# Kernel tuning notes

Hardware: AMD Instinct MI355X
Metric: run time of the kernel (lower is better)

Reference implementation:

```python
import jax, jax.numpy as jnp
import numpy as np

N = 512    # nnodes
H = 8      # attention heads
C = 32     # gnn_repr_size (per head)
ER = 32    # edge_repr_size
FE = 3     # feat_emb_size
E = 16384  # edges (avg degree 32)


def gat_conv(x, edge_index, edge_attr, W, att_src, att_dst, We, att_edge, b):
    """PyG GATConv (edge_dim=1, concat=True, add_self_loops=True, eval mode)."""
    n = x.shape[0]
    h_, c_ = att_src.shape
    row, col = edge_index[0], edge_index[1]
    # self loops with fill_value='mean': mean of incoming edge_attr per target node
    deg = jax.ops.segment_sum(jnp.ones_like(edge_attr), col, num_segments=n)
    loop_attr = jax.ops.segment_sum(edge_attr, col, num_segments=n) / jnp.maximum(deg, 1.0)
    ar = jnp.arange(n)
    row = jnp.concatenate([row, ar])
    col = jnp.concatenate([col, ar])
    ea = jnp.concatenate([edge_attr, loop_attr])
    # node projections [n, H, C]
    h = (x @ W.T).reshape(n, h_, c_)
    a_src = jnp.sum(h * att_src, axis=-1)  # [n, H]
    a_dst = jnp.sum(h * att_dst, axis=-1)  # [n, H]
    e = (ea[:, None] @ We.T).reshape(-1, h_, c_)  # [E', H, C]
    a_e = jnp.sum(e * att_edge, axis=-1)          # [E', H]
    alpha = jax.nn.leaky_relu(a_src[row] + a_dst[col] + a_e, 0.2)
    # softmax over edges grouped by destination node
    amax = jax.ops.segment_max(alpha, col, num_segments=n)
    ex = jnp.exp(alpha - amax[col])
    denom = jax.ops.segment_sum(ex, col, num_segments=n)
    alpha = ex / (denom[col] + 1e-16)
    out = jax.ops.segment_sum(h[row] * alpha[..., None], col, num_segments=n)
    return out.reshape(n, h_ * c_) + b


def setup_inputs():
    key = jax.random.key(0)
    ks = jax.random.split(key, 24)
    s = 0.05
    HC = H * C
    in_len = N * ER + 3 * N + 3 * FE  # combiner1 input length
    return {
        "dist": jax.random.uniform(ks[0], (N, N), dtype=jnp.float32),
        "markov": jax.random.uniform(ks[1], (N, N), dtype=jnp.float32),
        "demand": jax.random.normal(ks[2], (N,), dtype=jnp.float32),
        "W_week": jax.random.normal(ks[3], (7, FE)) * s,
        "W_cap": jax.random.normal(ks[4], (26, FE)) * s,
        "W_veh": jax.random.normal(ks[5], (15, FE)) * s,
        "g1_W": jax.random.normal(ks[6], (HC, 1)) * s,
        "g1_att_src": jax.random.normal(ks[7], (H, C)) * s,
        "g1_att_dst": jax.random.normal(ks[8], (H, C)) * s,
        "g1_We": jax.random.normal(ks[9], (HC, 1)) * s,
        "g1_att_edge": jax.random.normal(ks[10], (H, C)) * s,
        "g1_b": jnp.zeros((HC,), dtype=jnp.float32),
        "g2_W": jax.random.normal(ks[11], (HC, HC)) * s,
        "g2_att_src": jax.random.normal(ks[12], (H, C)) * s,
        "g2_att_dst": jax.random.normal(ks[13], (H, C)) * s,
        "g2_We": jax.random.normal(ks[14], (HC, 1)) * s,
        "g2_att_edge": jax.random.normal(ks[15], (H, C)) * s,
        "g2_b": jnp.zeros((HC,), dtype=jnp.float32),
        "Wes": jax.random.normal(ks[16], (ER, 2 * HC)) * s,
        "bes": jnp.zeros((ER,), dtype=jnp.float32),
        "Wc1": jax.random.normal(ks[17], (N, in_len)) * 0.01,
        "bc1": jnp.zeros((N,), dtype=jnp.float32),
        "Wc2": jax.random.normal(ks[18], (N, N)) * s,
        "bc2": jnp.zeros((N,), dtype=jnp.float32),
        "stops": jax.random.randint(ks[19], (256,), 0, N),
        "edge_index": jax.random.randint(ks[20], (2, E), 0, N),
        "weekday": 3,
        "vehicles": 7,
        "capacity": 12,
    }


def reference(dist, markov, demand, W_week, W_cap, W_veh,
              g1_W, g1_att_src, g1_att_dst, g1_We, g1_att_edge, g1_b,
              g2_W, g2_att_src, g2_att_dst, g2_We, g2_att_edge, g2_b,
              Wes, bes, Wc1, bc1, Wc2, bc2,
              stops, edge_index, weekday, vehicles, capacity):
    n = dist.shape[0]
    dist = (dist - dist.min()) / (dist.max() - dist.min())
    x = demand[:, None]  # [n, 1]
    ea = markov[edge_index[0], edge_index[1]]  # [E]
    x = jax.nn.relu(gat_conv(x, edge_index, ea, g1_W, g1_att_src, g1_att_dst, g1_We, g1_att_edge, g1_b))
    x = jax.nn.relu(gat_conv(x, edge_index, ea, g2_W, g2_att_src, g2_att_dst, g2_We, g2_att_edge, g2_b))
    HC_ = x.shape[1]
    # all-pairs edge representation: concat(x[i], x[j]) over meshgrid -> [n*n, 2*HC]
    er = jnp.concatenate([
        jnp.broadcast_to(x[:, None, :], (n, n, HC_)),
        jnp.broadcast_to(x[None, :, :], (n, n, HC_)),
    ], axis=-1).reshape(n * n, 2 * HC_)
    er = (er @ Wes.T + bes).reshape(n, -1)  # [n, n*ER]
    week = jnp.broadcast_to(W_week[weekday], (n, W_week.shape[1]))
    cap = jnp.broadcast_to(W_cap[capacity], (n, W_cap.shape[1]))
    veh = jnp.broadcast_to(W_veh[vehicles], (n, W_veh.shape[1]))
    stop = jnp.broadcast_to(jnp.zeros((n,), dtype=dist.dtype).at[stops].set(1.0)[None, :], (n, n))
    feat = jnp.concatenate([er, dist, markov, week, cap, veh, stop], axis=1)
    out = jax.nn.relu(feat @ Wc1.T + bc1) @ Wc2.T + bc2
    return out
```

## Files before the change

### kernel.cpp

```cpp
#include <hip/hip_runtime.h>
#include <hip/hip_bf16.h>

typedef __hip_bfloat16 bf16;
typedef __attribute__((ext_vector_type(8))) short bf16x8;
typedef __attribute__((ext_vector_type(4))) float f32x4;

#define NNODE 512
#define NEDGE 16384
#define INLEN 17929
#define K1P   1088

#define WS_EA      0
#define WS_CSRC    16384
#define WS_CEA     32768
#define WS_DEG     49152
#define WS_STARTS  49664
#define WS_LATTR   50176
#define WS_MM      50688
#define WS_MMP     50690
#define WS_STOPV   50818
#define WS_AE      51330
#define WS_PS      51346
#define WS_H       55552
#define WS_G2WT    186624
#define WS_H2      317696
#define WS_ASRC    448768
#define WS_ADST    452864
#define WS_UV      456960
#define WS_K       489728
#define WS_APACK   490240
#define WS_BPACK   768768
#define WS_OUT1    1047296
#define WS_WC2B    1178368
#define WS_WESF    1309440
#define WS_ASRC2   1325824
#define WS_ADST2   1329920
#define WS_CURSOR  1334016
#define WS_DEGP    1334528
#define WS_LSUMP   1367296
#define WS_OUT1F   1400064

static __device__ __forceinline__ unsigned short f2bfbits(float x){
  bf16 b = __float2bfloat16(x);
  union { bf16 b; unsigned short u; } c; c.b = b; return c.u;
}

__global__ __launch_bounds__(256)
void k_prep(const float* __restrict__ demand, const float* __restrict__ W1,
            const float* __restrict__ att_s, const float* __restrict__ att_d,
            const int* __restrict__ stops, const float* __restrict__ Wes,
            const float* __restrict__ dist, const float* __restrict__ markov,
            const int* __restrict__ eidx,
            const float* __restrict__ g1We, const float* __restrict__ g1ae,
            const float* __restrict__ g2We, const float* __restrict__ g2ae,
            const float* __restrict__ g2W,  const float* __restrict__ g2as,
            const float* __restrict__ g2ad, const float* __restrict__ Wc2,
            float* __restrict__ outp, float* ws){
  int b = blockIdx.x, tid = threadIdx.x;
  if (b < 512){
    int hd = tid>>5, c = tid&31;
    float hv = demand[b] * W1[tid];
    ws[WS_H + b*256 + tid] = hv;
    float ps = hv * att_s[tid];
    float pd = hv * att_d[tid];
    for (int off=16; off; off>>=1){ ps += __shfl_down(ps,off,32); pd += __shfl_down(pd,off,32); }
    if (c==0){ ws[WS_ASRC + b*8+hd]=ps; ws[WS_ADST + b*8+hd]=pd; }
  } else if (b == 512){
    ws[WS_STOPV+tid] = 0.f; ws[WS_STOPV+256+tid] = 0.f;
    __syncthreads();
    ws[WS_STOPV + stops[tid]] = 1.0f;
    if (tid < 8){
      float s=0.f; for (int c=0;c<32;c++) s += g1We[tid*32+c]*g1ae[tid*32+c];
      ws[WS_AE+tid]=s;
    } else if (tid < 16){
      int h=tid-8; float s=0.f; for (int c=0;c<32;c++) s += g2We[h*32+c]*g2ae[h*32+c];
      ws[WS_AE+8+h]=s;
    }
  } else if (b < 515){
    for (int idx = (b-513)*8192 + tid; idx < (b-512)*8192; idx += 256){
      int k = idx>>8, c = idx&255;
      ws[WS_WESF+idx] = (k<32) ? Wes[k*512+c] : Wes[(k-32)*512+256+c];
    }
  } else if (b < 579){
    __shared__ float smn[256], smx[256];
    int p = b-515;
    float mn = 3.4e38f, mx = -3.4e38f;
    const float4* dv = (const float4*)(dist + p*4096);
    #pragma unroll
    for (int k=0;k<4;k++){
      float4 v = dv[k*256 + tid];
      mn = fminf(mn, fminf(fminf(v.x,v.y), fminf(v.z,v.w)));
      mx = fmaxf(mx, fmaxf(fmaxf(v.x,v.y), fmaxf(v.z,v.w)));
    }
    smn[tid]=mn; smx[tid]=mx; __syncthreads();
    for (int off=128; off; off>>=1){
      if (tid<off){ smn[tid]=fminf(smn[tid],smn[tid+off]); smx[tid]=fmaxf(smx[tid],smx[tid+off]); }
      __syncthreads();
    }
    if (tid==0){ ws[WS_MMP+p]=smn[0]; ws[WS_MMP+64+p]=smx[0]; }
  } else if (b < 643){
    __shared__ int   hd_[512];
    __shared__ float hf_[512];
    int k = b-579;
    hd_[tid]=0; hd_[256+tid]=0; hf_[tid]=0.f; hf_[256+tid]=0.f;
    __syncthreads();
    int e = k*256 + tid;
    int r = eidx[e], c = eidx[NEDGE+e];
    float a = markov[r*NNODE + c];
    ws[WS_EA+e] = a;
    atomicAdd(&hd_[c], 1);
    atomicAdd(&hf_[c], a);
    __syncthreads();
    ((int*)(ws+WS_DEGP))[k*512+tid]     = hd_[tid];
    ((int*)(ws+WS_DEGP))[k*512+256+tid] = hd_[256+tid];
    ws[WS_LSUMP + k*512+tid]     = hf_[tid];
    ws[WS_LSUMP + k*512+256+tid] = hf_[256+tid];
  } else if (b < 659){
    int j = b-643;
    const float* att = (j<8) ? g2as : g2ad;
    int h = j&7;
    float s = 0.f;
    for (int c=0;c<32;c++) s += att[h*32+c] * g2W[(h*32+c)*256 + tid];
    ws[WS_PS + j*256 + tid] = s;
  } else if (b < 675){
    __shared__ float T[64][65];
    int tb = b-659, tr = tb>>2, tc = tb&3;
    int w = tid>>6, c = tid&63;
    for (int k=0;k<16;k++){
      int r = k*4 + w;
      T[r][c] = g2W[(tr*64+r)*256 + tc*64 + c];
    }
    __syncthreads();
    for (int k=0;k<16;k++){
      int r = k*4 + w;
      ws[WS_G2WT + (tc*64+r)*256 + tr*64 + c] = T[c][r];
    }
  } else if (b == 675){
    ((int*)(ws+WS_CURSOR))[tid] = 0;
    ((int*)(ws+WS_CURSOR))[256+tid] = 0;
  } else if (b < 740){
    int blk = b - 676;
    const float4* src = (const float4*)(Wc2 + blk*4096);
    ushort4* dst = (ushort4*)((unsigned short*)(ws+WS_WC2B) + blk*4096);
    #pragma unroll
    for (int i=0;i<4;i++){
      float4 v = src[i*256+tid];
      ushort4 u;
      u.x = f2bfbits(v.x); u.y = f2bfbits(v.y);
      u.z = f2bfbits(v.z); u.w = f2bfbits(v.w);
      dst[i*256+tid] = u;
    }
  } else {
    int blk = b - 740;
    float4 z = {0.f,0.f,0.f,0.f};
    float4* o1f = (float4*)(ws + WS_OUT1F);
    float4* op  = (float4*)outp;
    o1f[blk*512 + tid] = z;
    o1f[blk*512 + 256 + tid] = z;
    op[blk*512 + tid] = z;
    op[blk*512 + 256 + tid] = z;
  }
}

__global__ __launch_bounds__(512)
void k_scansc(const int* __restrict__ eidx, float* ws){
  __shared__ int sc[512];
  __shared__ int startS[512];
  __shared__ float rmn[64], rmx[64];
  int t = threadIdx.x, b = blockIdx.x;
  const int* dp = (const int*)(ws+WS_DEGP);
  int d = 0;
  for (int k=0;k<64;k++) d += dp[k*512+t];
  sc[t] = d; __syncthreads();
  for (int off=1; off<512; off<<=1){
    int v = (t>=off) ? sc[t-off] : 0; __syncthreads();
    sc[t] += v; __syncthreads();
  }
  startS[t] = sc[t]-d;
  if (b == 0){
    float l = 0.f;
    for (int k=0;k<64;k++) l += ws[WS_LSUMP+k*512+t];
    ((int*)(ws+WS_STARTS))[t] = startS[t];
    ((int*)(ws+WS_DEG))[t] = d;
    ws[WS_LATTR+t] = l / (float)(d>1 ? d : 1);
    if (t < 64){ rmn[t]=ws[WS_MMP+t]; rmx[t]=ws[WS_MMP+64+t]; }
    __syncthreads();
    if (t == 0){
      float mn=rmn[0], mx=rmx[0];
      for (int i=1;i<64;i++){ mn=fminf(mn,rmn[i]); mx=fmaxf(mx,rmx[i]); }
      ws[WS_MM]=mn; ws[WS_MM+1]=mx;
    }
  }
  __syncthreads();
  int e = b*512 + t;
  int c = eidx[NEDGE+e];
  int p = startS[c] + atomicAdd((int*)(ws+WS_CURSOR)+c, 1);
  ((int*)(ws+WS_CSRC))[p] = eidx[e];
  ws[WS_CEA+p] = ws[WS_EA+e];
}

template<int MODE>
__global__ __launch_bounds__(256)
void k_agg(const float* __restrict__ hbuf, const float* __restrict__ asrc,
           const float* __restrict__ adst, const int* __restrict__ csrc,
           const float* __restrict__ cea, const int* __restrict__ starts,
           const int* __restrict__ deg, const float* __restrict__ lattr,
           const float* __restrict__ AEp, const float* __restrict__ bvec,
           const float* __restrict__ dist, const float* __restrict__ markov,
           float* ws){
  int t = blockIdx.x, tid = threadIdx.x, hd = tid>>5;
  __shared__ int   srcE[256];
  __shared__ float eaE[256];
  __shared__ float Lall[256*8];
  __shared__ float AE[8], mh[8], dh[8], sw[8];
  __shared__ float xrow[256], uvrow[64];
  if (tid<8) AE[tid]=AEp[tid];
  __syncthreads();
  int d = deg[t], s0 = starts[t];
  if (d > 256) d = 256;
  for (int e=tid; e<d; e+=256){ srcE[e]=csrc[s0+e]; eaE[e]=cea[s0+e]; }
  __syncthreads();
  {
    int h8 = tid&7;
    float adt = adst[t*8+h8], aeh = AE[h8];
    for (int e = tid>>3; e < d; e += 32){
      float a = asrc[srcE[e]*8+h8] + adt + eaE[e]*aeh;
      Lall[e*8+h8] = a>=0.f ? a : 0.2f*a;
    }
  }
  __syncthreads();
  {
    int h = tid>>5, j = tid&31;
    float aself = asrc[t*8+h] + adst[t*8+h] + lattr[t]*AE[h];
    aself = aself>=0.f ? aself : 0.2f*aself;
    float mm = aself;
    for (int e=j; e<d; e+=32) mm = fmaxf(mm, Lall[e*8+h]);
    for (int off=16; off; off>>=1) mm = fmaxf(mm, __shfl_down(mm,off,32));
    mm = __shfl(mm, 0, 32);
    float dd = 0.f;
    for (int e=j; e<d; e+=32) dd += __expf(Lall[e*8+h]-mm);
    for (int off=16; off; off>>=1) dd += __shfl_down(dd,off,32);
    if (j==0){
      float se = __expf(aself-mm);
      mh[h]=mm; dh[h]=dd+se+1e-16f; sw[h]=se;
    }
  }
  __syncthreads();
  {
    int h8 = tid&7;
    for (int e = tid>>3; e < d; e += 32)
      Lall[e*8+h8] = __expf(Lall[e*8+h8] - mh[h8]);
  }
  __syncthreads();
  float a0 = sw[hd]*hbuf[t*256+tid], a1=0.f, a2=0.f, a3=0.f, a4=0.f, a5=0.f, a6=0.f, a7=0.f;
  int e = 0;
  for (; e+8<=d; e+=8){
    a0 += Lall[(e+0)*8+hd]*hbuf[srcE[e+0]*256+tid];
    a1 += Lall[(e+1)*8+hd]*hbuf[srcE[e+1]*256+tid];
    a2 += Lall[(e+2)*8+hd]*hbuf[srcE[e+2]*256+tid];
    a3 += Lall[(e+3)*8+hd]*hbuf[srcE[e+3]*256+tid];
    a4 += Lall[(e+4)*8+hd]*hbuf[srcE[e+4]*256+tid];
    a5 += Lall[(e+5)*8+hd]*hbuf[srcE[e+5]*256+tid];
    a6 += Lall[(e+6)*8+hd]*hbuf[srcE[e+6]*256+tid];
    a7 += Lall[(e+7)*8+hd]*hbuf[srcE[e+7]*256+tid];
  }
  for (; e<d; e++) a0 += Lall[e*8+hd]*hbuf[srcE[e]*256+tid];
  float v = fmaxf((((a0+a1)+(a2+a3))+((a4+a5)+(a6+a7)))/dh[hd] + bvec[tid], 0.f);
  xrow[tid] = v;
  __syncthreads();
  if (MODE == 1){
    const float* g2wt = ws + WS_G2WT;
    float h0=0.f,h1=0.f,h2=0.f,h3=0.f;
    for (int c=0;c<256;c+=4){
      h0 += xrow[c+0]*g2wt[(c+0)*256+tid];
      h1 += xrow[c+1]*g2wt[(c+1)*256+tid];
      h2 += xrow[c+2]*g2wt[(c+2)*256+tid];
      h3 += xrow[c+3]*g2wt[(c+3)*256+tid];
    }
    ws[WS_H2 + t*256 + tid] = (h0+h1)+(h2+h3);
    if (tid < 64){
      int j = tid>>2, q = tid&3;
      const float* pr = ws + WS_PS + j*256 + q*64;
      const float* xr = xrow + q*64;
      float p = 0.f;
      for (int c=0;c<64;c++) p += xr[c]*pr[c];
      p += __shfl_down(p,2,4);
      p += __shfl_down(p,1,4);
      if (q==0){
        if (j<8) ws[WS_ASRC2 + t*8+j] = p;
        else     ws[WS_ADST2 + t*8+(j-8)] = p;
      }
    }
  } else {
    int k = tid>>2, q = tid&3;
    const float* wr = ws + WS_WESF + k*256 + q*64;
    const float* xr = xrow + q*64;
    float p = 0.f;
    for (int c=0;c<64;c++) p += xr[c]*wr[c];
    p += __shfl_down(p,2,4);
    p += __shfl_down(p,1,4);
    if (q==0){ ws[WS_UV + t*64+k] = p; uvrow[k] = p; }
    __syncthreads();
    float mn = ws[WS_MM], mx = ws[WS_MM+1];
    float inv = 1.0f/(mx-mn);
    bf16* ap = (bf16*)(ws+WS_APACK);
    const float* mrow = markov + t*512;
    for (int j=tid; j<K1P; j+=256){
      float v2;
      if (j<32)        v2 = uvrow[j];
      else if (j<544)  v2 = (dist[t*512 + j-32] - mn) * inv;
      else if (j<1056) v2 = mrow[j-544];
      else             v2 = 0.f;
      ap[(size_t)t*K1P + j] = __float2bfloat16(v2);
    }
  }
}

__global__ __launch_bounds__(1024)
void k_skpack(const float* __restrict__ Wc1, const float* __restrict__ bc1,
              const float* __restrict__ bes, const float* __restrict__ Wweek,
              const float* __restrict__ Wcap, const float* __restrict__ Wveh,
              const int* __restrict__ wd, const int* __restrict__ vh,
              const int* __restrict__ cp, float* ws){
  int o = blockIdx.x, tid = threadIdx.x;
  __shared__ float besf[32];
  __shared__ float red[512];
  __shared__ float red2[16];
  if (tid<32) besf[tid] = bes[tid];
  __syncthreads();
  const float* wr = Wc1 + (size_t)o*INLEN;
  bf16* bp  = (bf16*)(ws+WS_BPACK);
  float be = besf[tid&31];
  const float* uvp = ws + WS_UV + ((tid>>5)<<6) + 32 + (tid&31);
  float sP = 0.f, tP0=0.f, tP1=0.f, tP2=0.f, tP3=0.f;
  #pragma unroll
  for (int i=0;i<16;i+=4){
    float w0 = wr[tid + 1024*(i+0)];
    float w1 = wr[tid + 1024*(i+1)];
    float w2 = wr[tid + 1024*(i+2)];
    float w3 = wr[tid + 1024*(i+3)];
    float u0 = uvp[2048*(i+0)];
    float u1 = uvp[2048*(i+1)];
    float u2 = uvp[2048*(i+2)];
    float u3 = uvp[2048*(i+3)];
    sP += (w0+w1)+(w2+w3);
    tP0 += w0*(u0+be);
    tP1 += w1*(u1+be);
    tP2 += w2*(u2+be);
    tP3 += w3*(u3+be);
  }
  float tP = (tP0+tP1)+(tP2+tP3);
  if (tid < 512) tP += ws[WS_STOPV+tid] * wr[17417+tid];
  if (tid < 9){
    int g = tid/3, f = tid-g*3;
    float sv = (g==0) ? Wweek[wd[0]*3+f]
             : (g==1) ? Wcap[cp[0]*3+f]
                      : Wveh[vh[0]*3+f];
    tP += sv * wr[17408+tid];
  }
  int lane = tid&63, w = tid>>6;
  sP += __shfl_down(sP, 32, 64);
  if (lane < 32) red[w*32 + lane] = sP;
  for (int off=32; off; off>>=1) tP += __shfl_down(tP, off, 64);
  if (lane == 0) red2[w] = tP;
  __syncthreads();
  if (tid < 32){
    float s = 0.f;
    #pragma unroll
    for (int k=0;k<16;k++) s += red[k*32+tid];
    bp[(size_t)o*K1P + tid] = __float2bfloat16(s);
    bp[(size_t)o*K1P + 1056 + tid] = __float2bfloat16(0.f);
  } else if (tid == 32){
    float s = 0.f;
    #pragma unroll
    for (int k=0;k<16;k++) s += red2[k];
    ws[WS_K+o] = s + bc1[o];
  }
  bp[(size_t)o*K1P + 32 + tid] = __float2bfloat16(wr[16384+tid]);
}

template<bool ADDB>
__global__ __launch_bounds__(512)
void gemm_split(const bf16* __restrict__ A, const bf16* __restrict__ B,
                const float* __restrict__ bias, float* __restrict__ C,
                int N, int K){
  __shared__ short Als[2][4096];
  __shared__ short Bls[2][4096];
  const int tid = threadIdx.x;
  const int bm = blockIdx.y*64, bn = blockIdx.x*64;
  const int kz = blockIdx.z, NS = gridDim.z;
  const int nkT = K>>6;
  const int kb = (nkT*kz)/NS, ke = (nkT*(kz+1))/NS, cnt = ke-kb;
  const int wave = tid>>6, lane = tid&63;
  const int wm = wave>>2, wn = wave&3;
  const int r = lane&15, q = lane>>4;
  f32x4 acc[2] = {};
  const int lrow = tid>>3, lk8 = tid&7;
  const bf16* Ag = A + (size_t)(bm+lrow)*K + kb*64 + lk8*8;
  const bf16* Bg = B + (size_t)(bn+lrow)*K + kb*64 + lk8*8;
  const int sidx = ((lk8>>2)*256 + (lk8&3)*64 + lrow)*8;
  float4 av = *(const float4*)(Ag);
  float4 bv = *(const float4*)(Bg);
  *(float4*)(&Als[0][sidx]) = av;
  *(float4*)(&Bls[0][sidx]) = bv;
  __syncthreads();
  for (int kk=0; kk<cnt; kk++){
    int cur = kk&1, nxt = cur^1;
    if (kk+1 < cnt){
      av = *(const float4*)(Ag + (kk+1)*64);
      bv = *(const float4*)(Bg + (kk+1)*64);
    }
    #pragma unroll
    for (int k2=0; k2<2; k2++){
      bf16x8 bfr = *(const bf16x8*)(&Bls[cur][(k2*256 + q*64 + wn*16 + r)*8]);
      #pragma unroll
      for (int i=0;i<2;i++){
        bf16x8 af = *(const bf16x8*)(&Als[cur][(k2*256 + q*64 + wm*32 + i*16 + r)*8]);
        acc[i] = __builtin_amdgcn_mfma_f32_16x16x32_bf16(af, bfr, acc[i], 0,0,0);
      }
    }
    if (kk+1 < cnt){
      __syncthreads();
      *(float4*)(&Als[nxt][sidx]) = av;
      *(float4*)(&Bls[nxt][sidx]) = bv;
      __syncthreads();
    }
  }
  const int col = bn + wn*16 + r;
  const float bi = (ADDB && kz==0) ? bias[col] : 0.f;
  #pragma unroll
  for (int i=0;i<2;i++){
    int row = bm + wm*32 + i*16 + q*4;
    #pragma unroll
    for (int g=0; g<4; g++)
      atomicAdd(&C[(size_t)(row+g)*N + col], acc[i][g] + bi);
  }
}

__global__ __launch_bounds__(256)
void k_ep1(float* ws){
  int idx = (blockIdx.x*256 + threadIdx.x)*8;
  const float4* s  = (const float4*)(ws + WS_OUT1F + idx);
  const float4* kv = (const float4*)(ws + WS_K + (idx&511));
  float4 v0 = s[0], v1 = s[1];
  float4 k0 = kv[0], k1 = kv[1];
  ushort4 u0, u1;
  u0.x = f2bfbits(fmaxf(v0.x+k0.x, 0.f));
  u0.y = f2bfbits(fmaxf(v0.y+k0.y, 0.f));
  u0.z = f2bfbits(fmaxf(v0.z+k0.z, 0.f));
  u0.w = f2bfbits(fmaxf(v0.w+k0.w, 0.f));
  u1.x = f2bfbits(fmaxf(v1.x+k1.x, 0.f));
  u1.y = f2bfbits(fmaxf(v1.y+k1.y, 0.f));
  u1.z = f2bfbits(fmaxf(v1.z+k1.z, 0.f));
  u1.w = f2bfbits(fmaxf(v1.w+k1.w, 0.f));
  ushort4* d = (ushort4*)((unsigned short*)(ws+WS_OUT1) + idx);
  d[0] = u0; d[1] = u1;
}

extern "C" void kernel_launch(void* const* d_in, const int* in_sizes, int n_in,
                              void* d_out, int out_size, void* d_ws, size_t ws_size,
                              hipStream_t stream){
  const float* dist   = (const float*)d_in[0];
  const float* markov = (const float*)d_in[1];
  const float* demand = (const float*)d_in[2];
  const float* Wweek  = (const float*)d_in[3];
  const float* Wcap   = (const float*)d_in[4];
  const float* Wveh   = (const float*)d_in[5];
  const float* g1W    = (const float*)d_in[6];
  const float* g1as   = (const float*)d_in[7];
  const float* g1ad   = (const float*)d_in[8];
  const float* g1We   = (const float*)d_in[9];
  const float* g1ae   = (const float*)d_in[10];
  const float* g1b    = (const float*)d_in[11];
  const float* g2W    = (const float*)d_in[12];
  const float* g2as   = (const float*)d_in[13];
  const float* g2ad   = (const float*)d_in[14];
  const float* g2We   = (const float*)d_in[15];
  const float* g2ae   = (const float*)d_in[16];
  const float* g2b    = (const float*)d_in[17];
  const float* Wes    = (const float*)d_in[18];
  const float* bes    = (const float*)d_in[19];
  const float* Wc1    = (const float*)d_in[20];
  const float* bc1    = (const float*)d_in[21];
  const float* Wc2    = (const float*)d_in[22];
  const float* bc2    = (const float*)d_in[23];
  const int*   stops  = (const int*)d_in[24];
  const int*   eidx   = (const int*)d_in[25];
  const int*   wd     = (const int*)d_in[26];
  const int*   vh     = (const int*)d_in[27];
  const int*   cp     = (const int*)d_in[28];
  float* out = (float*)d_out;
  float* ws = (float*)d_ws;

  const int*   csrc   = (const int*)(ws+WS_CSRC);
  const float* cea    = ws+WS_CEA;
  const int*   starts = (const int*)(ws+WS_STARTS);
  const int*   deg    = (const int*)(ws+WS_DEG);
  const float* lattr  = ws+WS_LATTR;

  k_prep<<<868,256,0,stream>>>(demand, g1W, g1as, g1ad, stops, Wes, dist, markov, eidx,
                               g1We, g1ae, g2We, g2ae, g2W, g2as, g2ad, Wc2, out, ws);
  k_scansc<<<32,512,0,stream>>>(eidx, ws);
  k_agg<1><<<512,256,0,stream>>>(ws+WS_H, ws+WS_ASRC, ws+WS_ADST, csrc, cea, starts, deg,
                                 lattr, ws+WS_AE, g1b, dist, markov, ws);
  k_agg<2><<<512,256,0,stream>>>(ws+WS_H2, ws+WS_ASRC2, ws+WS_ADST2, csrc, cea, starts, deg,
                                 lattr, ws+WS_AE+8, g2b, dist, markov, ws);
  k_skpack<<<512,1024,0,stream>>>(Wc1, bc1, bes, Wweek, Wcap, Wveh, wd, vh, cp, ws);
  gemm_split<false><<<dim3(8,8,4),512,0,stream>>>((const bf16*)(ws+WS_APACK), (const bf16*)(ws+WS_BPACK),
                                                  nullptr, ws+WS_OUT1F, 512, K1P);
  k_ep1<<<128,256,0,stream>>>(ws);
  gemm_split<true><<<dim3(8,8,2),512,0,stream>>>((const bf16*)(ws+WS_OUT1), (const bf16*)(ws+WS_WC2B),
                                                 bc2, out, 512, 512);
}
```

Before: 193.1 us.

## Exploit rank-1 first GAT layer, aggregate before projection, fuse epilogue into GEMM2

Because the first layer's input is a scalar per node, its aggregation becomes a per-head weighted sum of demand values times W1. This replaces the 256-wide gather over precomputed projections. The second layer now aggregates the layer-1 output first and applies the g2 projection afterwards in a new batched k_post kernel, which also computes the edge-repr projection and packs the A matrix. The scan uses wave shuffles instead of a shared-memory Hillis-Steele loop. The ReLU+bias+bf16 epilogue kernel is folded into the second GEMM's A load. This cuts launches and gather traffic but adds one kernel, and the rewritten first layer relies on the input projection having a single input feature.

```diff
diff --git a/kernel.cpp b/kernel.cpp
--- a/kernel.cpp
+++ b/kernel.cpp
@@ -21,16 +21,15 @@
 #define WS_STOPV   50818
 #define WS_AE      51330
 #define WS_PS      51346
-#define WS_H       55552
 #define WS_G2WT    186624
-#define WS_H2      317696
+#define WS_Y       317696
 #define WS_ASRC    448768
 #define WS_ADST    452864
 #define WS_UV      456960
 #define WS_K       489728
 #define WS_APACK   490240
 #define WS_BPACK   768768
-#define WS_OUT1    1047296
+#define WS_X1      1047296
 #define WS_WC2B    1178368
 #define WS_WESF    1309440
 #define WS_ASRC2   1325824
@@ -60,7 +59,6 @@
   if (b < 512){
     int hd = tid>>5, c = tid&31;
     float hv = demand[b] * W1[tid];
-    ws[WS_H + b*256 + tid] = hv;
     float ps = hv * att_s[tid];
     float pd = hv * att_d[tid];
     for (int off=16; off; off>>=1){ ps += __shfl_down(ps,off,32); pd += __shfl_down(pd,off,32); }
@@ -164,31 +162,37 @@
 
 __global__ __launch_bounds__(512)
 void k_scansc(const int* __restrict__ eidx, float* ws){
-  __shared__ int sc[512];
   __shared__ int startS[512];
-  __shared__ float rmn[64], rmx[64];
-  int t = threadIdx.x, b = blockIdx.x;
+  __shared__ int wsum[8];
+  int t = threadIdx.x, b = blockIdx.x, lane = t&63, w = t>>6;
   const int* dp = (const int*)(ws+WS_DEGP);
   int d = 0;
+  #pragma unroll 8
   for (int k=0;k<64;k++) d += dp[k*512+t];
-  sc[t] = d; __syncthreads();
-  for (int off=1; off<512; off<<=1){
-    int v = (t>=off) ? sc[t-off] : 0; __syncthreads();
-    sc[t] += v; __syncthreads();
-  }
-  startS[t] = sc[t]-d;
+  int v = d;
+  for (int off=1; off<64; off<<=1){
+    int u = __shfl_up(v, off, 64);
+    if (lane >= off) v += u;
+  }
+  if (lane==63) wsum[w] = v;
+  __syncthreads();
+  int base = 0;
+  for (int k=0;k<w;k++) base += wsum[k];
+  int incl = base + v;
+  startS[t] = incl - d;
   if (b == 0){
     float l = 0.f;
     for (int k=0;k<64;k++) l += ws[WS_LSUMP+k*512+t];
-    ((int*)(ws+WS_STARTS))[t] = startS[t];
+    ((int*)(ws+WS_STARTS))[t] = incl - d;
     ((int*)(ws+WS_DEG))[t] = d;
     ws[WS_LATTR+t] = l / (float)(d>1 ? d : 1);
-    if (t < 64){ rmn[t]=ws[WS_MMP+t]; rmx[t]=ws[WS_MMP+64+t]; }
-    __syncthreads();
-    if (t == 0){
-      float mn=rmn[0], mx=rmx[0];
-      for (int i=1;i<64;i++){ mn=fminf(mn,rmn[i]); mx=fmaxf(mx,rmx[i]); }
-      ws[WS_MM]=mn; ws[WS_MM+1]=mx;
+    if (t < 64){
+      float mn = ws[WS_MMP+t], mx = ws[WS_MMP+64+t];
+      for (int off=32; off; off>>=1){
+        mn = fminf(mn, __shfl_down(mn,off,64));
+        mx = fmaxf(mx, __shfl_down(mx,off,64));
+      }
+      if (t==0){ ws[WS_MM]=mn; ws[WS_MM+1]=mx; }
     }
   }
   __syncthreads();
@@ -201,24 +205,29 @@
 
 template<int MODE>
 __global__ __launch_bounds__(256)
-void k_agg(const float* __restrict__ hbuf, const float* __restrict__ asrc,
-           const float* __restrict__ adst, const int* __restrict__ csrc,
-           const float* __restrict__ cea, const int* __restrict__ starts,
-           const int* __restrict__ deg, const float* __restrict__ lattr,
-           const float* __restrict__ AEp, const float* __restrict__ bvec,
-           const float* __restrict__ dist, const float* __restrict__ markov,
+void k_agg(const float* __restrict__ asrc, const float* __restrict__ adst,
+           const float* __restrict__ AEp, const float* __restrict__ demand,
+           const float* __restrict__ w1, const float* __restrict__ b1,
            float* ws){
   int t = blockIdx.x, tid = threadIdx.x, hd = tid>>5;
   __shared__ int   srcE[256];
   __shared__ float eaE[256];
+  __shared__ float demE[256];
   __shared__ float Lall[256*8];
-  __shared__ float AE[8], mh[8], dh[8], sw[8];
-  __shared__ float xrow[256], uvrow[64];
+  __shared__ float AE[8], mh[8], dh[8], sw[8], sagg[8];
+  __shared__ float xrow[256];
   if (tid<8) AE[tid]=AEp[tid];
   __syncthreads();
-  int d = deg[t], s0 = starts[t];
+  const int* csrc = (const int*)(ws+WS_CSRC);
+  const float* cea = ws+WS_CEA;
+  int d  = ((const int*)(ws+WS_DEG))[t];
+  int s0 = ((const int*)(ws+WS_STARTS))[t];
   if (d > 256) d = 256;
-  for (int e=tid; e<d; e+=256){ srcE[e]=csrc[s0+e]; eaE[e]=cea[s0+e]; }
+  for (int e=tid; e<d; e+=256){
+    int s = csrc[s0+e];
+    srcE[e]=s; eaE[e]=cea[s0+e];
+    if (MODE==1) demE[e]=demand[s];
+  }
   __syncthreads();
   {
     int h8 = tid&7;
@@ -231,7 +240,7 @@
   __syncthreads();
   {
     int h = tid>>5, j = tid&31;
-    float aself = asrc[t*8+h] + adst[t*8+h] + lattr[t]*AE[h];
+    float aself = asrc[t*8+h] + adst[t*8+h] + ws[WS_LATTR+t]*AE[h];
     aself = aself>=0.f ? aself : 0.2f*aself;
     float mm = aself;
     for (int e=j; e<d; e+=32) mm = fmaxf(mm, Lall[e*8+h]);
@@ -252,63 +261,93 @@
       Lall[e*8+h8] = __expf(Lall[e*8+h8] - mh[h8]);
   }
   __syncthreads();
-  float a0 = sw[hd]*hbuf[t*256+tid], a1=0.f, a2=0.f, a3=0.f, a4=0.f, a5=0.f, a6=0.f, a7=0.f;
-  int e = 0;
-  for (; e+8<=d; e+=8){
-    a0 += Lall[(e+0)*8+hd]*hbuf[srcE[e+0]*256+tid];
-    a1 += Lall[(e+1)*8+hd]*hbuf[srcE[e+1]*256+tid];
-    a2 += Lall[(e+2)*8+hd]*hbuf[srcE[e+2]*256+tid];
-    a3 += Lall[(e+3)*8+hd]*hbuf[srcE[e+3]*256+tid];
-    a4 += Lall[(e+4)*8+hd]*hbuf[srcE[e+4]*256+tid];
-    a5 += Lall[(e+5)*8+hd]*hbuf[srcE[e+5]*256+tid];
-    a6 += Lall[(e+6)*8+hd]*hbuf[srcE[e+6]*256+tid];
-    a7 += Lall[(e+7)*8+hd]*hbuf[srcE[e+7]*256+tid];
-  }
-  for (; e<d; e++) a0 += Lall[e*8+hd]*hbuf[srcE[e]*256+tid];
-  float v = fmaxf((((a0+a1)+(a2+a3))+((a4+a5)+(a6+a7)))/dh[hd] + bvec[tid], 0.f);
-  xrow[tid] = v;
-  __syncthreads();
   if (MODE == 1){
-    const float* g2wt = ws + WS_G2WT;
-    float h0=0.f,h1=0.f,h2=0.f,h3=0.f;
-    for (int c=0;c<256;c+=4){
-      h0 += xrow[c+0]*g2wt[(c+0)*256+tid];
-      h1 += xrow[c+1]*g2wt[(c+1)*256+tid];
-      h2 += xrow[c+2]*g2wt[(c+2)*256+tid];
-      h3 += xrow[c+3]*g2wt[(c+3)*256+tid];
-    }
-    ws[WS_H2 + t*256 + tid] = (h0+h1)+(h2+h3);
+    int h = tid>>5, j = tid&31;
+    float s = 0.f;
+    for (int e=j; e<d; e+=32) s += Lall[e*8+h]*demE[e];
+    for (int off=16; off; off>>=1) s += __shfl_down(s,off,32);
+    if (j==0) sagg[h] = (s + sw[h]*demand[t]) / dh[h];
+    __syncthreads();
+    float v = fmaxf(sagg[hd]*w1[tid] + b1[tid], 0.f);
+    xrow[tid] = v;
+    ws[WS_X1 + t*256 + tid] = v;
+    __syncthreads();
     if (tid < 64){
-      int j = tid>>2, q = tid&3;
-      const float* pr = ws + WS_PS + j*256 + q*64;
+      int j2 = tid>>2, q = tid&3;
+      const float* pr = ws + WS_PS + j2*256 + q*64;
       const float* xr = xrow + q*64;
       float p = 0.f;
       for (int c=0;c<64;c++) p += xr[c]*pr[c];
       p += __shfl_down(p,2,4);
       p += __shfl_down(p,1,4);
       if (q==0){
-        if (j<8) ws[WS_ASRC2 + t*8+j] = p;
-        else     ws[WS_ADST2 + t*8+(j-8)] = p;
+        if (j2<8) ws[WS_ASRC2 + t*8+j2] = p;
+        else      ws[WS_ADST2 + t*8+(j2-8)] = p;
       }
     }
   } else {
-    int k = tid>>2, q = tid&3;
-    const float* wr = ws + WS_WESF + k*256 + q*64;
-    const float* xr = xrow + q*64;
+    const float* x1 = ws + WS_X1;
+    float a0 = sw[hd]*x1[t*256+tid], a1=0.f, a2=0.f, a3=0.f, a4=0.f, a5=0.f, a6=0.f, a7=0.f;
+    int e = 0;
+    for (; e+8<=d; e+=8){
+      a0 += Lall[(e+0)*8+hd]*x1[srcE[e+0]*256+tid];
+      a1 += Lall[(e+1)*8+hd]*x1[srcE[e+1]*256+tid];
+      a2 += Lall[(e+2)*8+hd]*x1[srcE[e+2]*256+tid];
+      a3 += Lall[(e+3)*8+hd]*x1[srcE[e+3]*256+tid];
+      a4 += Lall[(e+4)*8+hd]*x1[srcE[e+4]*256+tid];
+      a5 += Lall[(e+5)*8+hd]*x1[srcE[e+5]*256+tid];
+      a6 += Lall[(e+6)*8+hd]*x1[srcE[e+6]*256+tid];
+      a7 += Lall[(e+7)*8+hd]*x1[srcE[e+7]*256+tid];
+    }
+    for (; e<d; e++) a0 += Lall[e*8+hd]*x1[srcE[e]*256+tid];
+    ws[WS_Y + t*256 + tid] = (((a0+a1)+(a2+a3))+((a4+a5)+(a6+a7)))/dh[hd];
+  }
+}
+
+__global__ __launch_bounds__(256)
+void k_post(const float* __restrict__ dist, const float* __restrict__ markov,
+            const float* __restrict__ g2b, float* ws){
+  __shared__ float yls[4][256];
+  __shared__ float o2[4][256];
+  __shared__ float uvs[4][64];
+  int b = blockIdx.x, tid = threadIdx.x, n0 = b*4;
+  #pragma unroll
+  for (int n=0;n<4;n++) yls[n][tid] = ws[WS_Y + (n0+n)*256 + tid];
+  __syncthreads();
+  const float* T = ws + WS_G2WT;
+  float a0=0.f,a1=0.f,a2=0.f,a3=0.f;
+  #pragma unroll 4
+  for (int c=0;c<256;c++){
+    float w = T[c*256+tid];
+    a0 += yls[0][c]*w; a1 += yls[1][c]*w;
+    a2 += yls[2][c]*w; a3 += yls[3][c]*w;
+  }
+  float bb = g2b[tid];
+  o2[0][tid]=fmaxf(a0+bb,0.f); o2[1][tid]=fmaxf(a1+bb,0.f);
+  o2[2][tid]=fmaxf(a2+bb,0.f); o2[3][tid]=fmaxf(a3+bb,0.f);
+  __syncthreads();
+  {
+    int n = tid>>6, k = tid&63;
+    const float* wk = ws + WS_WESF + k*256;
     float p = 0.f;
-    for (int c=0;c<64;c++) p += xr[c]*wr[c];
-    p += __shfl_down(p,2,4);
-    p += __shfl_down(p,1,4);
-    if (q==0){ ws[WS_UV + t*64+k] = p; uvrow[k] = p; }
-    __syncthreads();
-    float mn = ws[WS_MM], mx = ws[WS_MM+1];
-    float inv = 1.0f/(mx-mn);
-    bf16* ap = (bf16*)(ws+WS_APACK);
+    #pragma unroll 4
+    for (int c=0;c<256;c++) p += o2[n][c]*wk[c];
+    uvs[n][k] = p;
+    ws[WS_UV + (n0+n)*64 + k] = p;
+  }
+  __syncthreads();
+  float mn = ws[WS_MM], mx = ws[WS_MM+1];
+  float inv = 1.0f/(mx-mn);
+  bf16* ap = (bf16*)(ws+WS_APACK);
+  #pragma unroll
+  for (int n=0;n<4;n++){
+    int t = n0+n;
+    const float* drow = dist + t*512;
     const float* mrow = markov + t*512;
     for (int j=tid; j<K1P; j+=256){
       float v2;
-      if (j<32)        v2 = uvrow[j];
-      else if (j<544)  v2 = (dist[t*512 + j-32] - mn) * inv;
+      if (j<32)        v2 = uvs[n][j];
+      else if (j<544)  v2 = (drow[j-32] - mn) * inv;
       else if (j<1056) v2 = mrow[j-544];
       else             v2 = 0.f;
       ap[(size_t)t*K1P + j] = __float2bfloat16(v2);
@@ -379,11 +418,9 @@
   bp[(size_t)o*K1P + 32 + tid] = __float2bfloat16(wr[16384+tid]);
 }
 
-template<bool ADDB>
 __global__ __launch_bounds__(512)
-void gemm_split(const bf16* __restrict__ A, const bf16* __restrict__ B,
-                const float* __restrict__ bias, float* __restrict__ C,
-                int N, int K){
+void gemm1_splitk(const bf16* __restrict__ A, const bf16* __restrict__ B,
+                  float* __restrict__ C, int N, int K){
   __shared__ short Als[2][4096];
   __shared__ short Bls[2][4096];
   const int tid = threadIdx.x;
@@ -427,34 +464,92 @@
     }
   }
   const int col = bn + wn*16 + r;
-  const float bi = (ADDB && kz==0) ? bias[col] : 0.f;
   #pragma unroll
   for (int i=0;i<2;i++){
     int row = bm + wm*32 + i*16 + q*4;
     #pragma unroll
     for (int g=0; g<4; g++)
+      atomicAdd(&C[(size_t)(row+g)*N + col], acc[i][g]);
+  }
+}
+
+__global__ __launch_bounds__(512)
+void gemm2_f32a(const float* __restrict__ Af, const bf16* __restrict__ B,
+                const float* __restrict__ kbias, const float* __restrict__ bc2,
+                float* __restrict__ C){
+  const int N = 512, K = 512;
+  __shared__ short Als[2][4096];
+  __shared__ short Bls[2][4096];
+  const int tid = threadIdx.x;
+  const int bm = blockIdx.y*64, bn = blockIdx.x*64;
+  const int kz = blockIdx.z, NS = gridDim.z;
+  const int nkT = K>>6;
+  const int kb = (nkT*kz)/NS, ke = (nkT*(kz+1))/NS, cnt = ke-kb;
+  const int wave = tid>>6, lane = tid&63;
+  const int wm = wave>>2, wn = wave&3;
+  const int r = lane&15, q = lane>>4;
+  f32x4 acc[2] = {};
+  const int lrow = tid>>3, lk8 = tid&7;
+  const float* Ag = Af + (size_t)(bm+lrow)*K + kb*64 + lk8*8;
+  const bf16*  Bg = B  + (size_t)(bn+lrow)*K + kb*64 + lk8*8;
+  const float* Kg = kbias + kb*64 + lk8*8;
+  const int sidx = ((lk8>>2)*256 + (lk8&3)*64 + lrow)*8;
+  union PK { ushort u[8]; float4 f; };
+  float4 x0, x1, k0, k1, bv;
+  auto loadA = [&](int kk){
+    x0 = *(const float4*)(Ag + kk*64);
+    x1 = *(const float4*)(Ag + kk*64 + 4);
+    k0 = *(const float4*)(Kg + kk*64);
+    k1 = *(const float4*)(Kg + kk*64 + 4);
+  };
+  auto packA = [&]()->float4 {
+    PK p;
+    p.u[0]=f2bfbits(fmaxf(x0.x+k0.x,0.f));
+    p.u[1]=f2bfbits(fmaxf(x0.y+k0.y,0.f));
+    p.u[2]=f2bfbits(fmaxf(x0.z+k0.z,0.f));
+    p.u[3]=f2bfbits(fmaxf(x0.w+k0.w,0.f));
+    p.u[4]=f2bfbits(fmaxf(x1.x+k1.x,0.f));
+    p.u[5]=f2bfbits(fmaxf(x1.y+k1.y,0.f));
+    p.u[6]=f2bfbits(fmaxf(x1.z+k1.z,0.f));
+    p.u[7]=f2bfbits(fmaxf(x1.w+k1.w,0.f));
+    return p.f;
+  };
+  loadA(0);
+  bv = *(const float4*)(Bg);
+  *(float4*)(&Als[0][sidx]) = packA();
+  *(float4*)(&Bls[0][sidx]) = bv;
+  __syncthreads();
+  for (int kk=0; kk<cnt; kk++){
+    int cur = kk&1, nxt = cur^1;
+    if (kk+1 < cnt){
+      loadA(kk+1);
+      bv = *(const float4*)(Bg + (kk+1)*64);
+    }
+    #pragma unroll
+    for (int k2=0; k2<2; k2++){
+      bf16x8 bfr = *(const bf16x8*)(&Bls[cur][(k2*256 + q*64 + wn*16 + r)*8]);
+      #pragma unroll
+      for (int i=0;i<2;i++){
+        bf16x8 af = *(const bf16x8*)(&Als[cur][(k2*256 + q*64 + wm*32 + i*16 + r)*8]);
+        acc[i] = __builtin_amdgcn_mfma_f32_16x16x32_bf16(af, bfr, acc[i], 0,0,0);
+      }
+    }
+    if (kk+1 < cnt){
+      __syncthreads();
+      *(float4*)(&Als[nxt][sidx]) = packA();
+      *(float4*)(&Bls[nxt][sidx]) = bv;
+      __syncthreads();
+    }
+  }
+  const int col = bn + wn*16 + r;
+  const float bi = (kz==0) ? bc2[col] : 0.f;
+  #pragma unroll
+  for (int i=0;i<2;i++){
+    int row = bm + wm*32 + i*16 + q*4;
+    #pragma unroll
+    for (int g=0; g<4; g++)
       atomicAdd(&C[(size_t)(row+g)*N + col], acc[i][g] + bi);
   }
-}
-
-__global__ __launch_bounds__(256)
-void k_ep1(float* ws){
-  int idx = (blockIdx.x*256 + threadIdx.x)*8;
-  const float4* s  = (const float4*)(ws + WS_OUT1F + idx);
-  const float4* kv = (const float4*)(ws + WS_K + (idx&511));
-  float4 v0 = s[0], v1 = s[1];
-  float4 k0 = kv[0], k1 = kv[1];
-  ushort4 u0, u1;
-  u0.x = f2bfbits(fmaxf(v0.x+k0.x, 0.f));
-  u0.y = f2bfbits(fmaxf(v0.y+k0.y, 0.f));
-  u0.z = f2bfbits(fmaxf(v0.z+k0.z, 0.f));
-  u0.w = f2bfbits(fmaxf(v0.w+k0.w, 0.f));
-  u1.x = f2bfbits(fmaxf(v1.x+k1.x, 0.f));
-  u1.y = f2bfbits(fmaxf(v1.y+k1.y, 0.f));
-  u1.z = f2bfbits(fmaxf(v1.z+k1.z, 0.f));
-  u1.w = f2bfbits(fmaxf(v1.w+k1.w, 0.f));
-  ushort4* d = (ushort4*)((unsigned short*)(ws+WS_OUT1) + idx);
-  d[0] = u0; d[1] = u1;
 }
 
 extern "C" void kernel_launch(void* const* d_in, const int* in_sizes, int n_in,
@@ -492,23 +587,15 @@
   float* out = (float*)d_out;
   float* ws = (float*)d_ws;
 
-  const int*   csrc   = (const int*)(ws+WS_CSRC);
-  const float* cea    = ws+WS_CEA;
-  const int*   starts = (const int*)(ws+WS_STARTS);
-  const int*   deg    = (const int*)(ws+WS_DEG);
-  const float* lattr  = ws+WS_LATTR;
-
   k_prep<<<868,256,0,stream>>>(demand, g1W, g1as, g1ad, stops, Wes, dist, markov, eidx,
                                g1We, g1ae, g2We, g2ae, g2W, g2as, g2ad, Wc2, out, ws);
   k_scansc<<<32,512,0,stream>>>(eidx, ws);
-  k_agg<1><<<512,256,0,stream>>>(ws+WS_H, ws+WS_ASRC, ws+WS_ADST, csrc, cea, starts, deg,
-                                 lattr, ws+WS_AE, g1b, dist, markov, ws);
-  k_agg<2><<<512,256,0,stream>>>(ws+WS_H2, ws+WS_ASRC2, ws+WS_ADST2, csrc, cea, starts, deg,
-                                 lattr, ws+WS_AE+8, g2b, dist, markov, ws);
+  k_agg<1><<<512,256,0,stream>>>(ws+WS_ASRC, ws+WS_ADST, ws+WS_AE, demand, g1W, g1b, ws);
+  k_agg<2><<<512,256,0,stream>>>(ws+WS_ASRC2, ws+WS_ADST2, ws+WS_AE+8, demand, g1W, g1b, ws);
+  k_post<<<128,256,0,stream>>>(dist, markov, g2b, ws);
   k_skpack<<<512,1024,0,stream>>>(Wc1, bc1, bes, Wweek, Wcap, Wveh, wd, vh, cp, ws);
-  gemm_split<false><<<dim3(8,8,4),512,0,stream>>>((const bf16*)(ws+WS_APACK), (const bf16*)(ws+WS_BPACK),
-                                                  nullptr, ws+WS_OUT1F, 512, K1P);
-  k_ep1<<<128,256,0,stream>>>(ws);
-  gemm_split<true><<<dim3(8,8,2),512,0,stream>>>((const bf16*)(ws+WS_OUT1), (const bf16*)(ws+WS_WC2B),
-                                                 bc2, out, 512, 512);
-}
+  gemm1_splitk<<<dim3(8,8,4),512,0,stream>>>((const bf16*)(ws+WS_APACK), (const bf16*)(ws+WS_BPACK),
+                                             ws+WS_OUT1F, 512, K1P);
+  gemm2_f32a<<<dim3(8,8,2),512,0,stream>>>(ws+WS_OUT1F, (const bf16*)(ws+WS_WC2B),
+                                           ws+WS_K, bc2, out);
+}
```

Measured after the change: 214.7 us. 11.2% more time.

## Exploit rank-1 first-layer features to aggregate scalars; use wave-shuffle scan

Applied to the files above, without the earlier changes.

The first GAT layer's input has one feature, so h = demand*W1. Aggregation then reduces to a per-head weighted sum of scalar demands followed by one multiply by W1. This removes the 256-wide gather over neighbour rows and the write of the h buffer in the prep kernel. The scan-and-scatter kernel also replaces its barrier-heavy shared-memory prefix scan and serial min/max reduction with wave shuffles. The rewrite reorders floating-point sums, so results may differ slightly from the reference.

```diff
diff --git a/kernel.cpp b/kernel.cpp
--- a/kernel.cpp
+++ b/kernel.cpp
@@ -21,7 +21,6 @@
 #define WS_STOPV   50818
 #define WS_AE      51330
 #define WS_PS      51346
-#define WS_H       55552
 #define WS_G2WT    186624
 #define WS_H2      317696
 #define WS_ASRC    448768
@@ -60,7 +59,6 @@
   if (b < 512){
     int hd = tid>>5, c = tid&31;
     float hv = demand[b] * W1[tid];
-    ws[WS_H + b*256 + tid] = hv;
     float ps = hv * att_s[tid];
     float pd = hv * att_d[tid];
     for (int off=16; off; off>>=1){ ps += __shfl_down(ps,off,32); pd += __shfl_down(pd,off,32); }
@@ -164,31 +162,37 @@
 
 __global__ __launch_bounds__(512)
 void k_scansc(const int* __restrict__ eidx, float* ws){
-  __shared__ int sc[512];
   __shared__ int startS[512];
-  __shared__ float rmn[64], rmx[64];
-  int t = threadIdx.x, b = blockIdx.x;
+  __shared__ int wsum[8];
+  int t = threadIdx.x, b = blockIdx.x, lane = t&63, w = t>>6;
   const int* dp = (const int*)(ws+WS_DEGP);
   int d = 0;
+  #pragma unroll 8
   for (int k=0;k<64;k++) d += dp[k*512+t];
-  sc[t] = d; __syncthreads();
-  for (int off=1; off<512; off<<=1){
-    int v = (t>=off) ? sc[t-off] : 0; __syncthreads();
-    sc[t] += v; __syncthreads();
-  }
-  startS[t] = sc[t]-d;
+  int v = d;
+  for (int off=1; off<64; off<<=1){
+    int u = __shfl_up(v, off, 64);
+    if (lane >= off) v += u;
+  }
+  if (lane==63) wsum[w] = v;
+  __syncthreads();
+  int base = 0;
+  for (int k=0;k<w;k++) base += wsum[k];
+  int incl = base + v;
+  startS[t] = incl - d;
   if (b == 0){
     float l = 0.f;
     for (int k=0;k<64;k++) l += ws[WS_LSUMP+k*512+t];
-    ((int*)(ws+WS_STARTS))[t] = startS[t];
+    ((int*)(ws+WS_STARTS))[t] = incl - d;
     ((int*)(ws+WS_DEG))[t] = d;
     ws[WS_LATTR+t] = l / (float)(d>1 ? d : 1);
-    if (t < 64){ rmn[t]=ws[WS_MMP+t]; rmx[t]=ws[WS_MMP+64+t]; }
-    __syncthreads();
-    if (t == 0){
-      float mn=rmn[0], mx=rmx[0];
-      for (int i=1;i<64;i++){ mn=fminf(mn,rmn[i]); mx=fmaxf(mx,rmx[i]); }
-      ws[WS_MM]=mn; ws[WS_MM+1]=mx;
+    if (t < 64){
+      float mn = ws[WS_MMP+t], mx = ws[WS_MMP+64+t];
+      for (int off=32; off; off>>=1){
+        mn = fminf(mn, __shfl_down(mn,off,64));
+        mx = fmaxf(mx, __shfl_down(mx,off,64));
+      }
+      if (t==0){ ws[WS_MM]=mn; ws[WS_MM+1]=mx; }
     }
   }
   __syncthreads();
@@ -202,23 +206,30 @@
 template<int MODE>
 __global__ __launch_bounds__(256)
 void k_agg(const float* __restrict__ hbuf, const float* __restrict__ asrc,
-           const float* __restrict__ adst, const int* __restrict__ csrc,
-           const float* __restrict__ cea, const int* __restrict__ starts,
-           const int* __restrict__ deg, const float* __restrict__ lattr,
-           const float* __restrict__ AEp, const float* __restrict__ bvec,
+           const float* __restrict__ adst, const float* __restrict__ AEp,
+           const float* __restrict__ bvec, const float* __restrict__ demand,
+           const float* __restrict__ w1,
            const float* __restrict__ dist, const float* __restrict__ markov,
            float* ws){
   int t = blockIdx.x, tid = threadIdx.x, hd = tid>>5;
   __shared__ int   srcE[256];
   __shared__ float eaE[256];
+  __shared__ float demE[256];
   __shared__ float Lall[256*8];
-  __shared__ float AE[8], mh[8], dh[8], sw[8];
+  __shared__ float AE[8], mh[8], dh[8], sw[8], sagg[8];
   __shared__ float xrow[256], uvrow[64];
   if (tid<8) AE[tid]=AEp[tid];
   __syncthreads();
-  int d = deg[t], s0 = starts[t];
+  const int* csrc = (const int*)(ws+WS_CSRC);
+  const float* cea = ws+WS_CEA;
+  int d  = ((const int*)(ws+WS_DEG))[t];
+  int s0 = ((const int*)(ws+WS_STARTS))[t];
   if (d > 256) d = 256;
-  for (int e=tid; e<d; e+=256){ srcE[e]=csrc[s0+e]; eaE[e]=cea[s0+e]; }
+  for (int e=tid; e<d; e+=256){
+    int s = csrc[s0+e];
+    srcE[e]=s; eaE[e]=cea[s0+e];
+    if (MODE==1) demE[e]=demand[s];
+  }
   __syncthreads();
   {
     int h8 = tid&7;
@@ -231,7 +242,7 @@
   __syncthreads();
   {
     int h = tid>>5, j = tid&31;
-    float aself = asrc[t*8+h] + adst[t*8+h] + lattr[t]*AE[h];
+    float aself = asrc[t*8+h] + adst[t*8+h] + ws[WS_LATTR+t]*AE[h];
     aself = aself>=0.f ? aself : 0.2f*aself;
     float mm = aself;
     for (int e=j; e<d; e+=32) mm = fmaxf(mm, Lall[e*8+h]);
@@ -252,23 +263,16 @@
       Lall[e*8+h8] = __expf(Lall[e*8+h8] - mh[h8]);
   }
   __syncthreads();
-  float a0 = sw[hd]*hbuf[t*256+tid], a1=0.f, a2=0.f, a3=0.f, a4=0.f, a5=0.f, a6=0.f, a7=0.f;
-  int e = 0;
-  for (; e+8<=d; e+=8){
-    a0 += Lall[(e+0)*8+hd]*hbuf[srcE[e+0]*256+tid];
-    a1 += Lall[(e+1)*8+hd]*hbuf[srcE[e+1]*256+tid];
-    a2 += Lall[(e+2)*8+hd]*hbuf[srcE[e+2]*256+tid];
-    a3 += Lall[(e+3)*8+hd]*hbuf[srcE[e+3]*256+tid];
-    a4 += Lall[(e+4)*8+hd]*hbuf[srcE[e+4]*256+tid];
-    a5 += Lall[(e+5)*8+hd]*hbuf[srcE[e+5]*256+tid];
-    a6 += Lall[(e+6)*8+hd]*hbuf[srcE[e+6]*256+tid];
-    a7 += Lall[(e+7)*8+hd]*hbuf[srcE[e+7]*256+tid];
-  }
-  for (; e<d; e++) a0 += Lall[e*8+hd]*hbuf[srcE[e]*256+tid];
-  float v = fmaxf((((a0+a1)+(a2+a3))+((a4+a5)+(a6+a7)))/dh[hd] + bvec[tid], 0.f);
-  xrow[tid] = v;
-  __syncthreads();
   if (MODE == 1){
+    int h = tid>>5, j = tid&31;
+    float s = 0.f;
+    for (int e=j; e<d; e+=32) s += Lall[e*8+h]*demE[e];
+    for (int off=16; off; off>>=1) s += __shfl_down(s,off,32);
+    if (j==0) sagg[h] = (s + sw[h]*demand[t]) / dh[h];
+    __syncthreads();
+    float v = fmaxf(sagg[hd]*w1[tid] + bvec[tid], 0.f);
+    xrow[tid] = v;
+    __syncthreads();
     const float* g2wt = ws + WS_G2WT;
     float h0=0.f,h1=0.f,h2=0.f,h3=0.f;
     for (int c=0;c<256;c+=4){
@@ -279,19 +283,35 @@
     }
     ws[WS_H2 + t*256 + tid] = (h0+h1)+(h2+h3);
     if (tid < 64){
-      int j = tid>>2, q = tid&3;
-      const float* pr = ws + WS_PS + j*256 + q*64;
+      int j2 = tid>>2, q = tid&3;
+      const float* pr = ws + WS_PS + j2*256 + q*64;
       const float* xr = xrow + q*64;
       float p = 0.f;
       for (int c=0;c<64;c++) p += xr[c]*pr[c];
       p += __shfl_down(p,2,4);
       p += __shfl_down(p,1,4);
       if (q==0){
-        if (j<8) ws[WS_ASRC2 + t*8+j] = p;
-        else     ws[WS_ADST2 + t*8+(j-8)] = p;
+        if (j2<8) ws[WS_ASRC2 + t*8+j2] = p;
+        else      ws[WS_ADST2 + t*8+(j2-8)] = p;
       }
     }
   } else {
+    float a0 = sw[hd]*hbuf[t*256+tid], a1=0.f, a2=0.f, a3=0.f, a4=0.f, a5=0.f, a6=0.f, a7=0.f;
+    int e = 0;
+    for (; e+8<=d; e+=8){
+      a0 += Lall[(e+0)*8+hd]*hbuf[srcE[e+0]*256+tid];
+      a1 += Lall[(e+1)*8+hd]*hbuf[srcE[e+1]*256+tid];
+      a2 += Lall[(e+2)*8+hd]*hbuf[srcE[e+2]*256+tid];
+      a3 += Lall[(e+3)*8+hd]*hbuf[srcE[e+3]*256+tid];
+      a4 += Lall[(e+4)*8+hd]*hbuf[srcE[e+4]*256+tid];
+      a5 += Lall[(e+5)*8+hd]*hbuf[srcE[e+5]*256+tid];
+      a6 += Lall[(e+6)*8+hd]*hbuf[srcE[e+6]*256+tid];
+      a7 += Lall[(e+7)*8+hd]*hbuf[srcE[e+7]*256+tid];
+    }
+    for (; e<d; e++) a0 += Lall[e*8+hd]*hbuf[srcE[e]*256+tid];
+    float v = fmaxf((((a0+a1)+(a2+a3))+((a4+a5)+(a6+a7)))/dh[hd] + bvec[tid], 0.f);
+    xrow[tid] = v;
+    __syncthreads();
     int k = tid>>2, q = tid&3;
     const float* wr = ws + WS_WESF + k*256 + q*64;
     const float* xr = xrow + q*64;
@@ -492,19 +512,13 @@
   float* out = (float*)d_out;
   float* ws = (float*)d_ws;
 
-  const int*   csrc   = (const int*)(ws+WS_CSRC);
-  const float* cea    = ws+WS_CEA;
-  const int*   starts = (const int*)(ws+WS_STARTS);
-  const int*   deg    = (const int*)(ws+WS_DEG);
-  const float* lattr  = ws+WS_LATTR;
-
   k_prep<<<868,256,0,stream>>>(demand, g1W, g1as, g1ad, stops, Wes, dist, markov, eidx,
                                g1We, g1ae, g2We, g2ae, g2W, g2as, g2ad, Wc2, out, ws);
   k_scansc<<<32,512,0,stream>>>(eidx, ws);
-  k_agg<1><<<512,256,0,stream>>>(ws+WS_H, ws+WS_ASRC, ws+WS_ADST, csrc, cea, starts, deg,
-                                 lattr, ws+WS_AE, g1b, dist, markov, ws);
-  k_agg<2><<<512,256,0,stream>>>(ws+WS_H2, ws+WS_ASRC2, ws+WS_ADST2, csrc, cea, starts, deg,
-                                 lattr, ws+WS_AE+8, g2b, dist, markov, ws);
+  k_agg<1><<<512,256,0,stream>>>(nullptr, ws+WS_ASRC, ws+WS_ADST, ws+WS_AE, g1b,
+                                 demand, g1W, dist, markov, ws);
+  k_agg<2><<<512,256,0,stream>>>(ws+WS_H2, ws+WS_ASRC2, ws+WS_ADST2, ws+WS_AE+8, g2b,
+                                 demand, g1W, dist, markov, ws);
   k_skpack<<<512,1024,0,stream>>>(Wc1, bc1, bes, Wweek, Wcap, Wveh, wd, vh, cp, ws);
   gemm_split<false><<<dim3(8,8,4),512,0,stream>>>((const bf16*)(ws+WS_APACK), (const bf16*)(ws+WS_BPACK),
                                                   nullptr, ws+WS_OUT1F, 512, K1P);
```

After: 191.3 us. Within noise of the previous version (-0.9%).
